# Kernel optimization log

Hardware: AMD Instinct MI355X
Metric: run time of the kernel (lower is better)

The kernel has to match this reference:

```python
import jax, jax.numpy as jnp
import numpy as np

D = 1024  # model_embedding_dim
T = 512   # n_future_dx
B = 16384


def setup_inputs() -> dict:
    key = jax.random.key(0)
    k1, k2, k3, k4, k5 = jax.random.split(key, 5)
    x = jax.random.normal(k1, (B, D), dtype=jnp.float32)
    # Linear layers: torch nn.Linear stores weight [out, in], bias [out]
    s = 1.0 / np.sqrt(D)
    Wh = jax.random.uniform(k2, (T, D), jnp.float32, -s, s)
    bh = jax.random.uniform(k3, (T,), jnp.float32, -s, s)
    Wb = jax.random.uniform(k4, (1, D), jnp.float32, -s, s)
    bb = jax.random.uniform(k5, (1,), jnp.float32, -s, s)
    return {"x": x, "Wh": Wh, "bh": bh, "Wb": Wb, "bb": bb}


def reference(x, Wh, bh, Wb, bb):
    # hazards = relu(x @ Wh^T + bh)  -> [B, T]
    hazards = jax.nn.relu(jnp.einsum('bd,td->bt', x, Wh) + bh)
    # masked expand-and-sum with upper-triangular mask (mask[i,j]=1 iff i<=j)
    # equals inclusive prefix sum along T.
    cum = jnp.cumsum(hazards, axis=1)
    base = jnp.einsum('bd,od->bo', x, Wb) + bb  # [B, 1]
    return cum + base
```

## Files before the change

kernel.cpp:

```cpp
#include <hip/hip_runtime.h>
#include <hip/hip_bf16.h>


typedef __bf16 bf16x8 __attribute__((ext_vector_type(8)));
typedef __bf16 bf16x4 __attribute__((ext_vector_type(4)));
typedef float f32x4 __attribute__((ext_vector_type(4)));

typedef const __attribute__((address_space(1))) void* gas_cptr;
typedef __attribute__((address_space(3))) void* las_ptr;

#define BM 64
#define BK 32
#define NKIT 32
#define TDIM 512
#define DDIM 1024
#define ASZ (BM * 64)
#define BSZ (TDIM * 64)

#define WAITV12()  asm volatile("s_waitcnt vmcnt(12) lgkmcnt(0)" ::: "memory")
#define WAITV6()   asm volatile("s_waitcnt vmcnt(6) lgkmcnt(0)"  ::: "memory")
#define WAITV0()   asm volatile("s_waitcnt vmcnt(0) lgkmcnt(0)"  ::: "memory")
#define WAIT_LGKM() asm volatile("s_waitcnt lgkmcnt(0)" ::: "memory")
#define SBAR()     __builtin_amdgcn_s_barrier()

__global__ __launch_bounds__(256) void cvt_wh_kernel(const float* __restrict__ src,
                                                     __bf16* __restrict__ dst) {
    const int i = (blockIdx.x * 256 + threadIdx.x) * 4;
    const float4 v = *reinterpret_cast<const float4*>(src + i);
    bf16x4 o;
    o[0] = (__bf16)v.x; o[1] = (__bf16)v.y; o[2] = (__bf16)v.z; o[3] = (__bf16)v.w;
    *reinterpret_cast<bf16x4*>(dst + i) = o;
}

__device__ __forceinline__ int swz64(int row) { return ((row >> 1) & 3) << 4; }

__global__ __launch_bounds__(512, 2) void survival_kernel(
    const float* __restrict__ x,
    const __bf16* __restrict__ Whb,
    const float* __restrict__ bh,
    const float* __restrict__ Wb,
    const float* __restrict__ bbp,
    float* __restrict__ out)
{
    __shared__ __align__(16) char Alds[3][ASZ];
    __shared__ __align__(16) char Blds[3][BSZ];
    __shared__ float baseLds[BM];
    __shared__ float totLds[BM][8];

    const int tid  = threadIdx.x;
    const int lane = tid & 63;
    const int wid  = tid >> 6;
    const int brow = blockIdx.x * BM;
    const float bb0 = bbp[0];

    const int ar = tid >> 3;
    const int ac = tid & 7;
    const float* xrow = x + (size_t)(brow + ar) * DDIM + ac * 4;
    const float* wbp  = Wb + ac * 4;
    const int a_off = ar * 64 + (((ac >> 1) * 16) ^ swz64(ar)) + (ac & 1) * 8;

    const int b_rbase = wid * 64 + (lane >> 2);
    const int b_slot  = lane & 3;

    float bpart = 0.f;
    f32x4 acc[4][4];
#pragma unroll
    for (int rt = 0; rt < 4; ++rt)
#pragma unroll
        for (int n = 0; n < 4; ++n)
            acc[rt][n] = (f32x4){0.f, 0.f, 0.f, 0.f};

    float4 xr0, wr0, xr1, wr1;

    auto issueT = [&](int buf, int it, int slot) {
        const int k0 = it * BK;
        if (slot == 0) { xr0 = *reinterpret_cast<const float4*>(xrow + k0);
                         wr0 = *reinterpret_cast<const float4*>(wbp + k0); }
        else           { xr1 = *reinterpret_cast<const float4*>(xrow + k0);
                         wr1 = *reinterpret_cast<const float4*>(wbp + k0); }
#pragma unroll
        for (int c = 0; c < 4; ++c) {
            const int row  = b_rbase + c * 16;
            const int colb = (b_slot * 16) ^ swz64(row);
            const __bf16* g = Whb + (size_t)row * DDIM + k0 + (colb >> 1);
            char* l = &Blds[buf][0] + (wid * 64 + c * 16) * 64;
            __builtin_amdgcn_global_load_lds((gas_cptr)(const void*)g,
                                             (las_ptr)(void*)l, 16, 0, 0);
        }
    };

    auto writeT = [&](int buf, int slot) {
        const float4 xv = slot ? xr1 : xr0;
        const float4 wv = slot ? wr1 : wr0;
        bpart += xv.x * wv.x + xv.y * wv.y + xv.z * wv.z + xv.w * wv.w;
        bf16x4 av;
        av[0] = (__bf16)xv.x; av[1] = (__bf16)xv.y;
        av[2] = (__bf16)xv.z; av[3] = (__bf16)xv.w;
        *reinterpret_cast<bf16x4*>(&Alds[buf][0] + a_off) = av;
    };

    auto compute = [&](int buf) {
        const char* Ab = &Alds[buf][0];
        const char* Bb = &Blds[buf][0];
        const int qslot = (lane >> 4) * 16;
        bf16x8 af[4];
#pragma unroll
        for (int rt = 0; rt < 4; ++rt) {
            const int row = rt * 16 + (lane & 15);
            af[rt] = *reinterpret_cast<const bf16x8*>(Ab + row * 64 + (qslot ^ swz64(row)));
        }
#pragma unroll
        for (int n = 0; n < 4; ++n) {
            const int trow = wid * 64 + n * 16 + (lane & 15);
            const bf16x8 bfr = *reinterpret_cast<const bf16x8*>(
                Bb + trow * 64 + (qslot ^ swz64(trow)));
#pragma unroll
            for (int rt = 0; rt < 4; ++rt)
                acc[rt][n] = __builtin_amdgcn_mfma_f32_16x16x32_bf16(af[rt], bfr, acc[rt][n], 0, 0, 0);
        }
    };

    issueT(0, 0, 0);
    issueT(1, 1, 1);
    writeT(0, 0);

#pragma unroll
    for (int t = 0; t < NKIT; ++t) {
        if (t + 2 < NKIT) issueT((t + 2) % 3, t + 2, t & 1);
        if (t + 2 < NKIT)      WAITV12();
        else if (t + 1 < NKIT) WAITV6();
        else                   WAITV0();
        SBAR();
        compute(t % 3);
        if (t + 1 < NKIT) writeT((t + 1) % 3, (t + 1) & 1);
        WAIT_LGKM();
        SBAR();
    }

    bpart += __shfl_xor(bpart, 1, 8);
    bpart += __shfl_xor(bpart, 2, 8);
    bpart += __shfl_xor(bpart, 4, 8);
    if (ac == 0) baseLds[ar] = bpart + bb0;

    float bhv[4];
#pragma unroll
    for (int n = 0; n < 4; ++n)
        bhv[n] = bh[wid * 64 + n * 16 + (lane & 15)];

    float carry[4][4];
#pragma unroll
    for (int rt = 0; rt < 4; ++rt)
#pragma unroll
        for (int j = 0; j < 4; ++j) carry[rt][j] = 0.f;

#pragma unroll
    for (int n = 0; n < 4; ++n) {
#pragma unroll
        for (int rt = 0; rt < 4; ++rt) {
#pragma unroll
            for (int j = 0; j < 4; ++j) {
                float v = fmaxf(acc[rt][n][j] + bhv[n], 0.f);
#pragma unroll
                for (int off = 1; off < 16; off <<= 1) {
                    const float u = __shfl_up(v, (unsigned)off, 16);
                    if ((lane & 15) >= off) v += u;
                }
                v += carry[rt][j];
                carry[rt][j] = __shfl(v, 15, 16);
                acc[rt][n][j] = v;
            }
        }
    }

    if ((lane & 15) == 0) {
#pragma unroll
        for (int rt = 0; rt < 4; ++rt)
#pragma unroll
            for (int j = 0; j < 4; ++j) {
                const int r = rt * 16 + (lane >> 4) * 4 + j;
                totLds[r][wid] = carry[rt][j];
            }
    }
    __syncthreads();

#pragma unroll
    for (int rt = 0; rt < 4; ++rt) {
#pragma unroll
        for (int j = 0; j < 4; ++j) {
            const int r = rt * 16 + (lane >> 4) * 4 + j;
            float rc = baseLds[r];
#pragma unroll
            for (int w = 0; w < 7; ++w)
                if (w < wid) rc += totLds[r][w];
            float* orow = out + (size_t)(brow + r) * TDIM + wid * 64 + (lane & 15);
#pragma unroll
            for (int n = 0; n < 4; ++n)
                orow[n * 16] = acc[rt][n][j] + rc;
        }
    }
}

extern "C" void kernel_launch(void* const* d_in, const int* in_sizes, int n_in,
                              void* d_out, int out_size, void* d_ws, size_t ws_size,
                              hipStream_t stream) {
    const float* x  = (const float*)d_in[0];
    const float* Wh = (const float*)d_in[1];
    const float* bh = (const float*)d_in[2];
    const float* Wb = (const float*)d_in[3];
    const float* bb = (const float*)d_in[4];
    float* out = (float*)d_out;
    __bf16* Whb = (__bf16*)d_ws;

    cvt_wh_kernel<<<512, 256, 0, stream>>>(Wh, Whb);
    survival_kernel<<<256, 512, 0, stream>>>(x, Whb, bh, Wb, bb, out);
}
```

Measured before the change: 151.4 us.

## Load Wh fragments directly from global and stage x in large K chunks

```diff
diff --git a/kernel.cpp b/kernel.cpp
--- a/kernel.cpp
+++ b/kernel.cpp
@@ -6,22 +6,13 @@
 typedef __bf16 bf16x4 __attribute__((ext_vector_type(4)));
 typedef float f32x4 __attribute__((ext_vector_type(4)));
 
-typedef const __attribute__((address_space(1))) void* gas_cptr;
-typedef __attribute__((address_space(3))) void* las_ptr;
-
 #define BM 64
-#define BK 32
-#define NKIT 32
+#define KC 256
+#define NCH 4
 #define TDIM 512
 #define DDIM 1024
-#define ASZ (BM * 64)
-#define BSZ (TDIM * 64)
-
-#define WAITV12()  asm volatile("s_waitcnt vmcnt(12) lgkmcnt(0)" ::: "memory")
-#define WAITV6()   asm volatile("s_waitcnt vmcnt(6) lgkmcnt(0)"  ::: "memory")
-#define WAITV0()   asm volatile("s_waitcnt vmcnt(0) lgkmcnt(0)"  ::: "memory")
-#define WAIT_LGKM() asm volatile("s_waitcnt lgkmcnt(0)" ::: "memory")
-#define SBAR()     __builtin_amdgcn_s_barrier()
+#define AROWB 512
+#define ACHSZ (BM * AROWB)
 
 __global__ __launch_bounds__(256) void cvt_wh_kernel(const float* __restrict__ src,
                                                      __bf16* __restrict__ dst) {
@@ -32,7 +23,9 @@
     *reinterpret_cast<bf16x4*>(dst + i) = o;
 }
 
-__device__ __forceinline__ int swz64(int row) { return ((row >> 1) & 3) << 4; }
+__device__ __forceinline__ int aswz(int row, int slotByte) {
+    return (slotByte ^ ((row & 7) << 4));
+}
 
 __global__ __launch_bounds__(512, 2) void survival_kernel(
     const float* __restrict__ x,
@@ -42,8 +35,7 @@
     const float* __restrict__ bbp,
     float* __restrict__ out)
 {
-    __shared__ __align__(16) char Alds[3][ASZ];
-    __shared__ __align__(16) char Blds[3][BSZ];
+    __shared__ __align__(16) char Alds[2][ACHSZ];
     __shared__ float baseLds[BM];
     __shared__ float totLds[BM][8];
 
@@ -55,12 +47,15 @@
 
     const int ar = tid >> 3;
     const int ac = tid & 7;
-    const float* xrow = x + (size_t)(brow + ar) * DDIM + ac * 4;
-    const float* wbp  = Wb + ac * 4;
-    const int a_off = ar * 64 + (((ac >> 1) * 16) ^ swz64(ar)) + (ac & 1) * 8;
-
-    const int b_rbase = wid * 64 + (lane >> 2);
-    const int b_slot  = lane & 3;
+    const float* xrow = x + (size_t)(brow + ar) * DDIM + ac * 32;
+    const float* wbp  = Wb + ac * 32;
+
+    const int tcol = lane & 15;
+    const int kq   = lane >> 4;
+    const __bf16* bbase[4];
+#pragma unroll
+    for (int n = 0; n < 4; ++n)
+        bbase[n] = Whb + (size_t)(wid * 64 + n * 16 + tcol) * DDIM + kq * 8;
 
     float bpart = 0.f;
     f32x4 acc[4][4];
@@ -70,71 +65,64 @@
         for (int n = 0; n < 4; ++n)
             acc[rt][n] = (f32x4){0.f, 0.f, 0.f, 0.f};
 
-    float4 xr0, wr0, xr1, wr1;
-
-    auto issueT = [&](int buf, int it, int slot) {
-        const int k0 = it * BK;
-        if (slot == 0) { xr0 = *reinterpret_cast<const float4*>(xrow + k0);
-                         wr0 = *reinterpret_cast<const float4*>(wbp + k0); }
-        else           { xr1 = *reinterpret_cast<const float4*>(xrow + k0);
-                         wr1 = *reinterpret_cast<const float4*>(wbp + k0); }
-#pragma unroll
-        for (int c = 0; c < 4; ++c) {
-            const int row  = b_rbase + c * 16;
-            const int colb = (b_slot * 16) ^ swz64(row);
-            const __bf16* g = Whb + (size_t)row * DDIM + k0 + (colb >> 1);
-            char* l = &Blds[buf][0] + (wid * 64 + c * 16) * 64;
-            __builtin_amdgcn_global_load_lds((gas_cptr)(const void*)g,
-                                             (las_ptr)(void*)l, 16, 0, 0);
-        }
+    float4 xs[8];
+
+    auto issueX = [&](int c) {
+#pragma unroll
+        for (int j = 0; j < 8; ++j)
+            xs[j] = *reinterpret_cast<const float4*>(xrow + c * KC + j * 4);
     };
 
-    auto writeT = [&](int buf, int slot) {
-        const float4 xv = slot ? xr1 : xr0;
-        const float4 wv = slot ? wr1 : wr0;
-        bpart += xv.x * wv.x + xv.y * wv.y + xv.z * wv.z + xv.w * wv.w;
-        bf16x4 av;
-        av[0] = (__bf16)xv.x; av[1] = (__bf16)xv.y;
-        av[2] = (__bf16)xv.z; av[3] = (__bf16)xv.w;
-        *reinterpret_cast<bf16x4*>(&Alds[buf][0] + a_off) = av;
+    auto writeA = [&](int c, int buf) {
+#pragma unroll
+        for (int j = 0; j < 8; ++j) {
+            const float4 wv = *reinterpret_cast<const float4*>(wbp + c * KC + j * 4);
+            bpart += xs[j].x * wv.x + xs[j].y * wv.y + xs[j].z * wv.z + xs[j].w * wv.w;
+        }
+#pragma unroll
+        for (int j2 = 0; j2 < 4; ++j2) {
+            bf16x8 av;
+            av[0] = (__bf16)xs[2*j2].x;   av[1] = (__bf16)xs[2*j2].y;
+            av[2] = (__bf16)xs[2*j2].z;   av[3] = (__bf16)xs[2*j2].w;
+            av[4] = (__bf16)xs[2*j2+1].x; av[5] = (__bf16)xs[2*j2+1].y;
+            av[6] = (__bf16)xs[2*j2+1].z; av[7] = (__bf16)xs[2*j2+1].w;
+            *reinterpret_cast<bf16x8*>(
+                &Alds[buf][0] + ar * AROWB + aswz(ar, (ac * 4 + j2) * 16)) = av;
+        }
     };
 
-    auto compute = [&](int buf) {
+    auto computeC = [&](int c, int buf) {
         const char* Ab = &Alds[buf][0];
-        const char* Bb = &Blds[buf][0];
-        const int qslot = (lane >> 4) * 16;
-        bf16x8 af[4];
-#pragma unroll
-        for (int rt = 0; rt < 4; ++rt) {
-            const int row = rt * 16 + (lane & 15);
-            af[rt] = *reinterpret_cast<const bf16x8*>(Ab + row * 64 + (qslot ^ swz64(row)));
-        }
-#pragma unroll
-        for (int n = 0; n < 4; ++n) {
-            const int trow = wid * 64 + n * 16 + (lane & 15);
-            const bf16x8 bfr = *reinterpret_cast<const bf16x8*>(
-                Bb + trow * 64 + (qslot ^ swz64(trow)));
-#pragma unroll
-            for (int rt = 0; rt < 4; ++rt)
-                acc[rt][n] = __builtin_amdgcn_mfma_f32_16x16x32_bf16(af[rt], bfr, acc[rt][n], 0, 0, 0);
+#pragma unroll
+        for (int kst = 0; kst < 8; ++kst) {
+            bf16x8 af[4];
+#pragma unroll
+            for (int rt = 0; rt < 4; ++rt) {
+                const int row = rt * 16 + tcol;
+                af[rt] = *reinterpret_cast<const bf16x8*>(
+                    Ab + row * AROWB + aswz(row, kst * 64 + kq * 16));
+            }
+#pragma unroll
+            for (int n = 0; n < 4; ++n) {
+                const bf16x8 bfr = *reinterpret_cast<const bf16x8*>(
+                    bbase[n] + c * KC + kst * 32);
+#pragma unroll
+                for (int rt = 0; rt < 4; ++rt)
+                    acc[rt][n] = __builtin_amdgcn_mfma_f32_16x16x32_bf16(
+                        af[rt], bfr, acc[rt][n], 0, 0, 0);
+            }
         }
     };
 
-    issueT(0, 0, 0);
-    issueT(1, 1, 1);
-    writeT(0, 0);
-
-#pragma unroll
-    for (int t = 0; t < NKIT; ++t) {
-        if (t + 2 < NKIT) issueT((t + 2) % 3, t + 2, t & 1);
-        if (t + 2 < NKIT)      WAITV12();
-        else if (t + 1 < NKIT) WAITV6();
-        else                   WAITV0();
-        SBAR();
-        compute(t % 3);
-        if (t + 1 < NKIT) writeT((t + 1) % 3, (t + 1) & 1);
-        WAIT_LGKM();
-        SBAR();
+    issueX(0);
+    writeA(0, 0);
+    __syncthreads();
+#pragma unroll
+    for (int c = 0; c < NCH; ++c) {
+        if (c + 1 < NCH) issueX(c + 1);
+        computeC(c, c & 1);
+        if (c + 1 < NCH) writeA(c + 1, (c + 1) & 1);
+        __syncthreads();
     }
 
     bpart += __shfl_xor(bpart, 1, 8);
@@ -145,7 +133,7 @@
     float bhv[4];
 #pragma unroll
     for (int n = 0; n < 4; ++n)
-        bhv[n] = bh[wid * 64 + n * 16 + (lane & 15)];
+        bhv[n] = bh[wid * 64 + n * 16 + tcol];
 
     float carry[4][4];
 #pragma unroll
@@ -172,12 +160,12 @@
         }
     }
 
-    if ((lane & 15) == 0) {
+    if (tcol == 0) {
 #pragma unroll
         for (int rt = 0; rt < 4; ++rt)
 #pragma unroll
             for (int j = 0; j < 4; ++j) {
-                const int r = rt * 16 + (lane >> 4) * 4 + j;
+                const int r = rt * 16 + kq * 4 + j;
                 totLds[r][wid] = carry[rt][j];
             }
     }
@@ -187,12 +175,12 @@
     for (int rt = 0; rt < 4; ++rt) {
 #pragma unroll
         for (int j = 0; j < 4; ++j) {
-            const int r = rt * 16 + (lane >> 4) * 4 + j;
+            const int r = rt * 16 + kq * 4 + j;
             float rc = baseLds[r];
 #pragma unroll
             for (int w = 0; w < 7; ++w)
                 if (w < wid) rc += totLds[r][w];
-            float* orow = out + (size_t)(brow + r) * TDIM + wid * 64 + (lane & 15);
+            float* orow = out + (size_t)(brow + r) * TDIM + wid * 64 + tcol;
 #pragma unroll
             for (int n = 0; n < 4; ++n)
                 orow[n * 16] = acc[rt][n][j] + rc;
```

Result: slower. 156.7 us (+3.5%).
